# Kernel tuning notes

Measured on AMD Instinct MI355X. Metric: run time of the kernel, lower is better.

Reference implementation:

```python
import jax, jax.numpy as jnp
import numpy as np

MARGIN = 2.0


def setup_inputs() -> dict:
    key = jax.random.key(0)
    k1, k2 = jax.random.split(key)
    B, D, NUM_CLASSES = 8192, 128, 100
    features = jax.random.normal(k1, (B, D), dtype=jnp.float32)
    labels = jax.random.randint(k2, (B,), 0, NUM_CLASSES, dtype=jnp.int64)
    return {"features": features, "labels": labels}


def reference(features, labels):
    # Vectorized form of the O(B^2) nested-loop contrastive loss.
    B = features.shape[0]
    sq = jnp.sum(features * features, axis=-1)                      # [B]
    # squared pairwise L2 distances via the gram matrix
    d2 = sq[:, None] + sq[None, :] - 2.0 * (features @ features.T)  # [B, B]
    d2 = jnp.maximum(d2, 0.0)

    off_diag = ~jnp.eye(B, dtype=bool)
    same = labels[:, None] == labels[None, :]
    pos_mask = same & off_diag
    neg_mask = (~same) & off_diag

    # positive pairs contribute squared distance
    pos_loss = jnp.sum(jnp.where(pos_mask, d2, 0.0))

    # negative pairs contribute clamp(margin - dist, 0)^2; guard sqrt(0) grads
    d = jnp.sqrt(jnp.where(neg_mask, d2, 1.0))
    hinge = jnp.maximum(MARGIN - d, 0.0)
    neg_loss = jnp.sum(jnp.where(neg_mask, hinge * hinge, 0.0))

    pos_count = jnp.sum(pos_mask)
    total_pairs = jnp.asarray(B * (B - 1), dtype=d2.dtype)
    loss = pos_loss + neg_loss
    # original divides only when positive_pairs > 0
    return jnp.where(pos_count > 0, loss / total_pairs, loss)
```

## Files before the change

kernel.cpp:

```cpp
#include <hip/hip_runtime.h>
#include <hip/hip_bf16.h>


#define BN 8192
#define DD 128
#define NTILES 64
#define NBLOCKS (NTILES * (NTILES + 1) / 2)
#define SQ 26.0f
#define INV_S2 (1.0f / (26.0f * 26.0f))

typedef __attribute__((ext_vector_type(4))) int i32x4;

__global__ __launch_bounds__(256) void prep_kernel(const float* __restrict__ f,
        const int* __restrict__ labels, char* __restrict__ fbp,
        int2* __restrict__ meta) {
    const int tid = threadIdx.x;
    const int p = blockIdx.x;
    __shared__ __align__(16) char ls[16][144];

    const int r = tid >> 4;
    const int c = (tid & 15) * 8;
    const float* src = f + ((size_t)p * 16 + r) * DD + c;
    float4 a = *(const float4*)src;
    float4 b = *(const float4*)(src + 4);
    float rv[8] = {a.x, a.y, a.z, a.w, b.x, b.y, b.z, b.w};
    int s = 0;
#pragma unroll
    for (int j = 0; j < 8; j++) {
        int q = __float2int_rn(fminf(fmaxf(rv[j] * SQ, -127.f), 127.f));
        ls[r][c + j] = (char)q;
        s += q * q;
    }
#pragma unroll
    for (int off = 8; off > 0; off >>= 1) s += __shfl_down(s, off, 16);
    if ((tid & 15) == 0) meta[p * 16 + r] = make_int2(s, labels[p * 16 + r]);
    __syncthreads();

    if (tid < 128) {
        const int ks = tid >> 6, lane = tid & 63;
        const int l15 = lane & 15, quad = lane >> 4;
        i32x4 pack = *(const i32x4*)&ls[l15][ks * 64 + quad * 16];
        *(i32x4*)(fbp + ((size_t)(p * 2 + ks) * 64 + lane) * 16) = pack;
    }
}

__global__ __launch_bounds__(256) void pair_kernel(
        const char* __restrict__ fbp, const int2* __restrict__ meta,
        float2* __restrict__ partial) {
    const int t = blockIdx.x;
    int by = (int)((sqrtf(8.f * (float)t + 1.f) - 1.f) * 0.5f);
    while ((by + 1) * (by + 2) / 2 <= t) by++;
    while (by * (by + 1) / 2 > t) by--;
    const int bx = t - by * (by + 1) / 2;
    const bool diag = (bx == by);

    const int tid = threadIdx.x;
    const int wave = tid >> 6, lane = tid & 63;
    const int wx = wave & 1, wy = wave >> 1;
    const int i0 = bx * 128 + wy * 64;
    const int j0 = by * 128 + wx * 64;
    const int ip = i0 >> 4, jp = j0 >> 4;
    const int l15 = lane & 15, quad = lane >> 4;

    float pos = 0.f, neg = 0.f;

    if (!(diag && wx < wy)) {
        i32x4 acc4[4][4];
#pragma unroll
        for (int a = 0; a < 4; a++)
#pragma unroll
            for (int b = 0; b < 4; b++) acc4[a][b] = (i32x4){0, 0, 0, 0};

#pragma unroll
        for (int ks = 0; ks < 2; ks++) {
            i32x4 af[4], bg[4];
#pragma unroll
            for (int tt = 0; tt < 4; tt++)
                af[tt] = *(const i32x4*)(fbp +
                    ((size_t)((ip + tt) * 2 + ks) * 64 + lane) * 16);
#pragma unroll
            for (int tt = 0; tt < 4; tt++)
                bg[tt] = *(const i32x4*)(fbp +
                    ((size_t)((jp + tt) * 2 + ks) * 64 + lane) * 16);
#pragma unroll
            for (int m = 0; m < 4; m++)
#pragma unroll
                for (int n = 0; n < 4; n++)
                    acc4[m][n] = __builtin_amdgcn_mfma_i32_16x16x64_i8(
                        af[m], bg[n], acc4[m][n], 0, 0, 0);
        }

        int2 mj[4];
#pragma unroll
        for (int ni = 0; ni < 4; ni++) mj[ni] = meta[j0 + ni * 16 + l15];
        int2 mi[4][4];
#pragma unroll
        for (int m = 0; m < 4; m++)
#pragma unroll
            for (int r = 0; r < 4; r++) mi[m][r] = meta[i0 + m * 16 + quad * 4 + r];

        const bool strict = diag && (wx == wy);
#pragma unroll
        for (int m = 0; m < 4; m++)
#pragma unroll
            for (int n = 0; n < 4; n++)
#pragma unroll
                for (int r = 0; r < 4; r++) {
                    int il = m * 16 + quad * 4 + r;
                    int jl = n * 16 + l15;
                    bool valid = !strict || (il < jl);
                    int d2i = mi[m][r].x + mj[n].x - 2 * acc4[m][n][r];
                    float d2 = (float)d2i * INV_S2;
                    if (valid) {
                        if (mi[m][r].y == mj[n].y) pos += d2;
                        else if (d2 < 4.0f) {
                            float h = 2.0f - sqrtf(d2);
                            neg += h * h;
                        }
                    }
                }
    }

#pragma unroll
    for (int off = 32; off > 0; off >>= 1) {
        pos += __shfl_down(pos, off, 64);
        neg += __shfl_down(neg, off, 64);
    }
    __shared__ float red[2][4];
    if (lane == 0) { red[0][wave] = pos; red[1][wave] = neg; }
    __syncthreads();
    if (tid == 0)
        partial[t] = make_float2(red[0][0] + red[0][1] + red[0][2] + red[0][3],
                                 red[1][0] + red[1][1] + red[1][2] + red[1][3]);
}

__global__ __launch_bounds__(256) void reduce_kernel(
        const float2* __restrict__ partial, float* __restrict__ out) {
    const int tid = threadIdx.x;
    float p = 0.f, n = 0.f;
    for (int i = tid; i < NBLOCKS; i += 256) {
        float2 v = partial[i];
        p += v.x; n += v.y;
    }
#pragma unroll
    for (int off = 32; off > 0; off >>= 1) {
        p += __shfl_down(p, off, 64);
        n += __shfl_down(n, off, 64);
    }
    __shared__ float red[2][4];
    int lane = tid & 63, w = tid >> 6;
    if (lane == 0) { red[0][w] = p; red[1][w] = n; }
    __syncthreads();
    if (tid == 0) {
        float total = 2.0f * (red[0][0] + red[0][1] + red[0][2] + red[0][3] +
                              red[1][0] + red[1][1] + red[1][2] + red[1][3]);
        out[0] = total / 67100672.0f;
    }
}

extern "C" void kernel_launch(void* const* d_in, const int* in_sizes, int n_in,
                              void* d_out, int out_size, void* d_ws, size_t ws_size,
                              hipStream_t stream) {
    const float* f = (const float*)d_in[0];
    const int* labels = (const int*)d_in[1];
    float* out = (float*)d_out;

    char* fbp = (char*)d_ws;
    int2* meta = (int2*)((char*)d_ws + (size_t)BN * DD);
    float2* partial = (float2*)(meta + BN);

    prep_kernel<<<BN / 16, 256, 0, stream>>>(f, labels, fbp, meta);
    pair_kernel<<<NBLOCKS, 256, 0, stream>>>(fbp, meta, partial);
    reduce_kernel<<<1, 256, 0, stream>>>(partial, out);
}
```

Baseline: 84.93 us.

## Factor positive-pair norms out of pair loop via per-class counts in reduce

The positive-pair sum is split algebraically. The squared-norm terms become sum_i |x_i|^2*(count[label_i]-1), computed in the reduce kernel from a shared-memory class histogram, while the pair kernel only accumulates integer dot products for same-label pairs. The negative-pair test now compares against an integer margin threshold, so the float conversion and sqrt are skipped for pairs that fail it. This trims per-element ALU work in the hot epilogue. In exchange the single-block reduce kernel grows to 1024 threads and must scan all 8192 rows, and the histogram hardcodes 100 classes.

```diff
diff --git a/kernel.cpp b/kernel.cpp
--- a/kernel.cpp
+++ b/kernel.cpp
@@ -8,6 +8,7 @@
 #define NBLOCKS (NTILES * (NTILES + 1) / 2)
 #define SQ 26.0f
 #define INV_S2 (1.0f / (26.0f * 26.0f))
+#define MARGIN2_I 2704
 
 typedef __attribute__((ext_vector_type(4))) int i32x4;
 
@@ -62,7 +63,7 @@
     const int ip = i0 >> 4, jp = j0 >> 4;
     const int l15 = lane & 15, quad = lane >> 4;
 
-    float pos = 0.f, neg = 0.f;
+    float posdot = 0.f, neg = 0.f;
 
     if (!(diag && wx < wy)) {
         i32x4 acc4[4][4];
@@ -100,6 +101,7 @@
             for (int r = 0; r < 4; r++) mi[m][r] = meta[i0 + m * 16 + quad * 4 + r];
 
         const bool strict = diag && (wx == wy);
+        int pd = 0;
 #pragma unroll
         for (int m = 0; m < 4; m++)
 #pragma unroll
@@ -109,51 +111,67 @@
                     int il = m * 16 + quad * 4 + r;
                     int jl = n * 16 + l15;
                     bool valid = !strict || (il < jl);
-                    int d2i = mi[m][r].x + mj[n].x - 2 * acc4[m][n][r];
-                    float d2 = (float)d2i * INV_S2;
-                    if (valid) {
-                        if (mi[m][r].y == mj[n].y) pos += d2;
-                        else if (d2 < 4.0f) {
-                            float h = 2.0f - sqrtf(d2);
+                    int dot = acc4[m][n][r];
+                    bool same = (mi[m][r].y == mj[n].y);
+                    if (valid && same) pd += dot;
+                    else if (valid) {
+                        int d2i = mi[m][r].x + mj[n].x - 2 * dot;
+                        if (d2i < MARGIN2_I) {
+                            float h = 2.0f - sqrtf((float)d2i * INV_S2);
                             neg += h * h;
                         }
                     }
                 }
+        posdot = (float)pd;
     }
 
 #pragma unroll
     for (int off = 32; off > 0; off >>= 1) {
-        pos += __shfl_down(pos, off, 64);
+        posdot += __shfl_down(posdot, off, 64);
         neg += __shfl_down(neg, off, 64);
     }
     __shared__ float red[2][4];
-    if (lane == 0) { red[0][wave] = pos; red[1][wave] = neg; }
+    if (lane == 0) { red[0][wave] = posdot; red[1][wave] = neg; }
     __syncthreads();
     if (tid == 0)
         partial[t] = make_float2(red[0][0] + red[0][1] + red[0][2] + red[0][3],
                                  red[1][0] + red[1][1] + red[1][2] + red[1][3]);
 }
 
-__global__ __launch_bounds__(256) void reduce_kernel(
-        const float2* __restrict__ partial, float* __restrict__ out) {
+__global__ __launch_bounds__(1024) void reduce_kernel(
+        const int2* __restrict__ meta, const float2* __restrict__ partial,
+        float* __restrict__ out) {
     const int tid = threadIdx.x;
-    float p = 0.f, n = 0.f;
-    for (int i = tid; i < NBLOCKS; i += 256) {
+    __shared__ int cnt[100];
+    if (tid < 100) cnt[tid] = 0;
+    __syncthreads();
+    for (int i = tid; i < BN; i += 1024) atomicAdd(&cnt[meta[i].y], 1);
+    __syncthreads();
+
+    float g = 0.f, p = 0.f, n = 0.f;
+    for (int i = tid; i < BN; i += 1024) {
+        int2 m = meta[i];
+        g += (float)m.x * (float)(cnt[m.y] - 1);
+    }
+    for (int i = tid; i < NBLOCKS; i += 1024) {
         float2 v = partial[i];
         p += v.x; n += v.y;
     }
 #pragma unroll
     for (int off = 32; off > 0; off >>= 1) {
+        g += __shfl_down(g, off, 64);
         p += __shfl_down(p, off, 64);
         n += __shfl_down(n, off, 64);
     }
-    __shared__ float red[2][4];
+    __shared__ float red[3][16];
     int lane = tid & 63, w = tid >> 6;
-    if (lane == 0) { red[0][w] = p; red[1][w] = n; }
+    if (lane == 0) { red[0][w] = g; red[1][w] = p; red[2][w] = n; }
     __syncthreads();
     if (tid == 0) {
-        float total = 2.0f * (red[0][0] + red[0][1] + red[0][2] + red[0][3] +
-                              red[1][0] + red[1][1] + red[1][2] + red[1][3]);
+        float G = 0.f, P = 0.f, N = 0.f;
+#pragma unroll
+        for (int i = 0; i < 16; i++) { G += red[0][i]; P += red[1][i]; N += red[2][i]; }
+        float total = (2.0f * G - 4.0f * P) * INV_S2 + 2.0f * N;
         out[0] = total / 67100672.0f;
     }
 }
@@ -171,5 +189,5 @@
 
     prep_kernel<<<BN / 16, 256, 0, stream>>>(f, labels, fbp, meta);
     pair_kernel<<<NBLOCKS, 256, 0, stream>>>(fbp, meta, partial);
-    reduce_kernel<<<1, 256, 0, stream>>>(partial, out);
+    reduce_kernel<<<1, 1024, 0, stream>>>(meta, partial, out);
 }
```

Measured after the change: 95.16 us. 12.1% more time.
